# Kernel tuning notes

Measured on AMD Instinct MI355X. Metric: run time of the kernel, lower is better.

Reference implementation:

```python
import jax, jax.numpy as jnp
import numpy as np

DILATIONS = [1, 2, 4]


def _lstm_cell(x, h, c, W_ih, W_hh, b_ih, b_hh):
    # PyTorch LSTMCell: gates in i, f, g, o order
    gates = x @ W_ih.T + b_ih + h @ W_hh.T + b_hh
    i, f, g, o = jnp.split(gates, 4, axis=-1)
    c_new = jax.nn.sigmoid(f) * c + jax.nn.sigmoid(i) * jnp.tanh(g)
    h_new = jax.nn.sigmoid(o) * jnp.tanh(c_new)
    return h_new, c_new


def _drnn_forward(x, params):
    B, T, _ = x.shape
    H = params[0][1].shape[1]
    L = len(params)
    # static per-(t, layer) update mask from dilations
    masks = jnp.asarray(
        np.array([[t % d == 0 for d in DILATIONS] for t in range(T)], dtype=bool)
    )  # [T, L]

    hs0 = tuple(jnp.zeros((B, H), x.dtype) for _ in range(L))
    cs0 = tuple(jnp.zeros((B, H), x.dtype) for _ in range(L))

    def step(carry, inp):
        hs, cs = carry
        x_t, m = inp  # x_t: [B, F], m: [L] bool
        hs = list(hs)
        cs = list(cs)
        for l, (Wi, Wh, bi, bh) in enumerate(params):
            inp_l = x_t if l == 0 else hs[l - 1]
            h_new, c_new = _lstm_cell(inp_l, hs[l], cs[l], Wi, Wh, bi, bh)
            hs[l] = jnp.where(m[l], h_new, hs[l])
            cs[l] = jnp.where(m[l], c_new, cs[l])
        return (tuple(hs), tuple(cs)), hs[-1]

    _, ys = jax.lax.scan(step, (hs0, cs0), (jnp.swapaxes(x, 0, 1), masks))
    return jnp.swapaxes(ys, 0, 1)  # [B, T, H]


def setup_inputs() -> dict:
    key = jax.random.key(0)
    ks = jax.random.split(key, 16)
    B, T, F, H = 128, 1024, 128, 256
    k = 1.0 / np.sqrt(H)  # torch LSTMCell init scale

    def u(kk, shape):
        return jax.random.uniform(kk, shape, jnp.float32, -k, k)

    inp = {"x": jax.random.normal(ks[0], (B, T, F), jnp.float32)}
    in_sizes = [F, H, H]
    ki = 1
    for l in range(3):
        inp[f"W_ih{l}"] = u(ks[ki], (4 * H, in_sizes[l])); ki += 1
        inp[f"W_hh{l}"] = u(ks[ki], (4 * H, H)); ki += 1
        inp[f"b_ih{l}"] = u(ks[ki], (4 * H,)); ki += 1
        inp[f"b_hh{l}"] = u(ks[ki], (4 * H,)); ki += 1
    return inp


def reference(x, W_ih0, W_hh0, b_ih0, b_hh0,
              W_ih1, W_hh1, b_ih1, b_hh1,
              W_ih2, W_hh2, b_ih2, b_hh2):
    params = [
        (W_ih0, W_hh0, b_ih0, b_hh0),
        (W_ih1, W_hh1, b_ih1, b_hh1),
        (W_ih2, W_hh2, b_ih2, b_hh2),
    ]
    return _drnn_forward(x, params)
```

## Files before the change

kernel.cpp:

```cpp
#include <hip/hip_runtime.h>
#include <hip/hip_fp16.h>
#include <stdint.h>
#include <stddef.h>


typedef _Float16 f16;
typedef _Float16 v2h __attribute__((ext_vector_type(2)));
typedef _Float16 v8h __attribute__((ext_vector_type(8)));
typedef __fp16 h2_raw __attribute__((ext_vector_type(2)));
typedef __fp16 h8_raw __attribute__((ext_vector_type(8)));
typedef float v4f __attribute__((ext_vector_type(4)));
typedef unsigned long long u64;

#define DEVINL static __device__ __forceinline__

DEVINL float sigm(float x) { return 1.0f / (1.0f + __expf(-x)); }
DEVINL float tanh_(float x) {
  x = fminf(fmaxf(x, -15.0f), 15.0f);
  float e = __expf(-2.0f * x);
  return (1.0f - e) / (1.0f + e);
}
DEVINL v2h pack2(float a, float b) {
  return __builtin_bit_cast(v2h, __builtin_amdgcn_cvt_pkrtz(a, b));
}
DEVINL v2h bcast_pair(v2h v, int l) {
  int i = __builtin_bit_cast(int, v);
  i = __builtin_amdgcn_readlane(i, l);
  return __builtin_bit_cast(v2h, i);
}
DEVINL float fdot2(v2h a, v2h b, float c) {
  return __builtin_amdgcn_fdot2(__builtin_bit_cast(h2_raw, a),
                                __builtin_bit_cast(h2_raw, b), c, false);
}
DEVINL v4f mfma_16x16x32(v8h a, v8h b, v4f c) {
  return __builtin_amdgcn_mfma_f32_16x16x32_f16(__builtin_bit_cast(h8_raw, a),
                                                __builtin_bit_cast(h8_raw, b), c,
                                                0, 0, 0);
}


__global__ void k_cvt_x(const float2* __restrict__ src, v2h* __restrict__ dst, int n2) {
  int i = blockIdx.x * blockDim.x + threadIdx.x;
  int st = gridDim.x * blockDim.x;
  for (; i < n2; i += st) {
    float2 v = src[i];
    dst[i] = pack2(v.x, v.y);
  }
}

__global__ void k_prep_w(const float* __restrict__ wih0, const float* __restrict__ whh0,
                         const float* __restrict__ wih1, const float* __restrict__ whh1,
                         const float* __restrict__ wih2, const float* __restrict__ whh2,
                         const float* __restrict__ bi0, const float* __restrict__ bh0,
                         const float* __restrict__ bi1, const float* __restrict__ bh1,
                         const float* __restrict__ bi2, const float* __restrict__ bh2,
                         f16* wih0f, f16* whh0f, f16* wih1f, f16* whh1f,
                         f16* wih2f, f16* whh2f,
                         float* bias0, float* bias1, float* bias2) {
  int i = blockIdx.x * blockDim.x + threadIdx.x;
  if (i < 131072) wih0f[i] = (f16)wih0[i];
  whh0f[i] = (f16)whh0[i];
  wih1f[i] = (f16)wih1[i];
  whh1f[i] = (f16)whh1[i];
  wih2f[i] = (f16)wih2[i];
  whh2f[i] = (f16)whh2[i];
  if (i < 1024) {
    bias0[i] = bi0[i] + bh0[i];
    bias1[i] = bi1[i] + bh1[i];
    bias2[i] = bi2[i] + bh2[i];
  }
}


template <int K>
__launch_bounds__(256)
__global__ void k_gemm(const f16* __restrict__ A, int Tb, int t0,
                       const f16* __restrict__ W, const float* __restrict__ bias,
                       f16* __restrict__ G) {
  constexpr int LDK = K + 8;
  __shared__ f16 As[64 * LDK];
  int b = blockIdx.x >> 2, tb = blockIdx.x & 3;
  const f16* Ablk = A + ((size_t)b * Tb + t0 + tb * 64) * K;
  int tid = threadIdx.x;

  constexpr int NV = 64 * K / 8;
  const uint4* src = (const uint4*)Ablk;
  for (int i = tid; i < NV; i += 256) {
    int e = i * 8;
    int r = e / K, c0 = e % K;
    *(uint4*)&As[r * LDK + c0] = src[i];
  }
  __syncthreads();

  int wave = tid >> 6, lane = tid & 63;
  int lm = lane & 15, lk = (lane >> 4) * 8;

  v8h af[K / 32];
#pragma unroll
  for (int kc = 0; kc < K / 32; ++kc)
    af[kc] = *(const v8h*)&As[(wave * 16 + lm) * LDK + kc * 32 + lk];

  size_t grow0 = (size_t)b * 256 + tb * 64 + wave * 16;
  for (int nt = 0; nt < 64; ++nt) {
    v4f acc = {0.0f, 0.0f, 0.0f, 0.0f};
    const f16* Wrow = W + (size_t)(nt * 16 + lm) * K + lk;
#pragma unroll
    for (int kc = 0; kc < K / 32; ++kc) {
      v8h bf = *(const v8h*)(Wrow + kc * 32);
      acc = mfma_16x16x32(af[kc], bf, acc);
    }
    float bv = bias[nt * 16 + lm];
#pragma unroll
    for (int r = 0; r < 4; ++r) {
      int m = (lane >> 4) * 4 + r;
      G[(grow0 + m) * 1024 + nt * 16 + lm] = (f16)(acc[r] + bv);
    }
  }
}


template <int LAYER>
__launch_bounds__(512, 2)
__global__ void k_rec(const f16* __restrict__ G,
                      const f16* __restrict__ Whh,
                      int t0, int steps,
                      f16* __restrict__ Hout, float* __restrict__ y,
                      float* __restrict__ hstate, float* __restrict__ cstate,
                      u64* hxw) {
  int blk = blockIdx.x;
  int b = blk >> 1, half = blk & 1;
  int tid = threadIdx.x;
  int lane = tid & 63;
  int g = tid >> 7, j = tid & 127;
  int col = g * 256 + half * 128 + j;

  __shared__ float gbuf[512];
  __shared__ uint32_t hbufw[64];

  v2h w0[64], w1[64];
  {
    const v8h* wown = (const v8h*)(Whh + (size_t)col * 256 + half * 128);
    const v8h* woth = (const v8h*)(Whh + (size_t)col * 256 + (1 - half) * 128);
#pragma unroll
    for (int i = 0; i < 16; ++i) {
      v8h qa = wown[i], qb = woth[i];
#pragma unroll
      for (int p = 0; p < 4; ++p) {
        v2h ta, tb;
        ta[0] = qa[2 * p]; ta[1] = qa[2 * p + 1];
        tb[0] = qb[2 * p]; tb[1] = qb[2 * p + 1];
        w0[i * 4 + p] = ta;
        w1[i * 4 + p] = tb;
      }
    }
  }

  u64* myw = hxw + (size_t)(b * 2 + half) * 128;
  const u64* pw = hxw + (size_t)(b * 2 + (1 - half)) * 128;

  float c_st = 0.0f, last_h = 0.0f;
  v2h hp_own = pack2(0.0f, 0.0f), hp_oth = pack2(0.0f, 0.0f);

  if (t0 > 0) {
    float2 a = *(const float2*)&hstate[b * 256 + half * 128 + 2 * lane];
    hp_own = pack2(a.x, a.y);
    if (tid < 128) {
      last_h = hstate[b * 256 + half * 128 + tid];
      c_st = cstate[b * 256 + half * 128 + tid];
    }
  }

  const f16* Gp = G + (size_t)b * 256 * 1024 + col;
  float gcur = (float)Gp[0];

  for (int s = 0; s < steps; ++s) {
    int t = t0 + s;

    const u64* pwp = pw + (((t - 1) & 1) << 6) + lane;
    u64 wp = 0;
    if (t > 0)
      wp = __hip_atomic_load(pwp, __ATOMIC_RELAXED, __HIP_MEMORY_SCOPE_AGENT);
    float gnext = (s + 1 < steps) ? (float)Gp[(size_t)(s + 1) << 10] : 0.0f;

    float acc = gcur;
#pragma unroll
    for (int kk = 0; kk < 64; ++kk)
      acc = fdot2(w0[kk], bcast_pair(hp_own, kk), acc);

    if (t > 0) {
      while ((int)(wp >> 32) < t)
        wp = __hip_atomic_load(pwp, __ATOMIC_RELAXED, __HIP_MEMORY_SCOPE_AGENT);
      hp_oth = __builtin_bit_cast(v2h, (uint32_t)wp);
    }

#pragma unroll
    for (int kk = 0; kk < 64; ++kk)
      acc = fdot2(w1[kk], bcast_pair(hp_oth, kk), acc);

    gbuf[tid] = acc;
    __syncthreads();

    if (tid < 128) {
      float iv = sigm(gbuf[tid]);
      float fv = sigm(gbuf[tid + 128]);
      float gv = tanh_(gbuf[tid + 256]);
      float ov = sigm(gbuf[tid + 384]);
      c_st = fv * c_st + iv * gv;
      float hnew = ov * tanh_(c_st);
      last_h = hnew;
      float hn1 = __shfl_down(hnew, 1, 64);
      if ((tid & 1) == 0) {
        uint32_t pk = __builtin_bit_cast(uint32_t, pack2(hnew, hn1));
        u64 wv = ((u64)(uint32_t)(t + 1) << 32) | (u64)pk;
        __hip_atomic_store(&myw[((t & 1) << 6) + (tid >> 1)], wv,
                           __ATOMIC_RELAXED, __HIP_MEMORY_SCOPE_AGENT);
        hbufw[tid >> 1] = pk;
      }
      if (LAYER == 0) {
        if ((t & 1) == 0)
          Hout[((size_t)b * 512 + (t >> 1)) * 256 + half * 128 + tid] = (f16)hnew;
      } else if (LAYER == 1) {
        if ((t & 1) == 0)
          Hout[((size_t)b * 256 + (t >> 1)) * 256 + half * 128 + tid] = (f16)hnew;
      } else {
        size_t base = ((size_t)b * 1024 + (size_t)t * 4) * 256 + half * 128 + tid;
        y[base] = hnew;
        y[base + 256] = hnew;
        y[base + 512] = hnew;
        y[base + 768] = hnew;
      }
    }
    __syncthreads();
    hp_own = __builtin_bit_cast(v2h, hbufw[lane]);
    gcur = gnext;
  }

  if (tid < 128) {
    hstate[b * 256 + half * 128 + tid] = last_h;
    cstate[b * 256 + half * 128 + tid] = c_st;
  }
}


extern "C" void kernel_launch(void* const* d_in, const int* in_sizes, int n_in,
                              void* d_out, int out_size, void* d_ws, size_t ws_size,
                              hipStream_t stream) {
  const float* x = (const float*)d_in[0];
  const float* wih[3] = {(const float*)d_in[1], (const float*)d_in[5], (const float*)d_in[9]};
  const float* whh[3] = {(const float*)d_in[2], (const float*)d_in[6], (const float*)d_in[10]};
  const float* bi[3] = {(const float*)d_in[3], (const float*)d_in[7], (const float*)d_in[11]};
  const float* bh[3] = {(const float*)d_in[4], (const float*)d_in[8], (const float*)d_in[12]};
  float* y = (float*)d_out;

  char* p = (char*)d_ws;
  f16* Xf = (f16*)p;        p += (size_t)16777216 * 2;
  f16* Wih0f = (f16*)p;     p += (size_t)131072 * 2;
  f16* Whh0f = (f16*)p;     p += (size_t)262144 * 2;
  f16* Wih1f = (f16*)p;     p += (size_t)262144 * 2;
  f16* Whh1f = (f16*)p;     p += (size_t)262144 * 2;
  f16* Wih2f = (f16*)p;     p += (size_t)262144 * 2;
  f16* Whh2f = (f16*)p;     p += (size_t)262144 * 2;
  float* bias0 = (float*)p; p += 4096;
  float* bias1 = (float*)p; p += 4096;
  float* bias2 = (float*)p; p += 4096;
  f16* Gbuf = (f16*)p;      p += (size_t)32768 * 1024 * 2;
  f16* H0e = (f16*)p;       p += (size_t)128 * 512 * 256 * 2;
  f16* H1q = (f16*)p;       p += (size_t)128 * 256 * 256 * 2;
  float* hstate = (float*)p; p += (size_t)128 * 256 * 4;
  float* cstate = (float*)p; p += (size_t)128 * 256 * 4;
  u64* hxw0 = (u64*)p;      p += (size_t)128 * 2 * 128 * 8;
  u64* hxw1 = (u64*)p;      p += (size_t)128 * 2 * 128 * 8;
  u64* hxw2 = (u64*)p;      p += (size_t)128 * 2 * 128 * 8;

  k_cvt_x<<<4096, 256, 0, stream>>>((const float2*)x, (v2h*)Xf, 8388608);
  k_prep_w<<<1024, 256, 0, stream>>>(wih[0], whh[0], wih[1], whh[1], wih[2], whh[2],
                                     bi[0], bh[0], bi[1], bh[1], bi[2], bh[2],
                                     Wih0f, Whh0f, Wih1f, Whh1f, Wih2f, Whh2f,
                                     bias0, bias1, bias2);

  for (int c = 0; c < 4; ++c) {
    k_gemm<128><<<512, 256, 0, stream>>>(Xf, 1024, c * 256, Wih0f, bias0, Gbuf);
    k_rec<0><<<256, 512, 0, stream>>>(Gbuf, Whh0f, c * 256, 256, H0e, nullptr,
                                      hstate, cstate, hxw0);
  }
  for (int c = 0; c < 2; ++c) {
    k_gemm<256><<<512, 256, 0, stream>>>(H0e, 512, c * 256, Wih1f, bias1, Gbuf);
    k_rec<1><<<256, 512, 0, stream>>>(Gbuf, Whh1f, c * 256, 256, H1q, nullptr,
                                      hstate, cstate, hxw1);
  }
  k_gemm<256><<<512, 256, 0, stream>>>(H1q, 256, 0, Wih2f, bias2, Gbuf);
  k_rec<2><<<256, 512, 0, stream>>>(Gbuf, Whh2f, 0, 256, nullptr, y,
                                    hstate, cstate, hxw2);
}
```

Measured before the change: 4.740 ms.

## Compute LSTM cell redundantly per wave to drop second barrier per step

```diff
diff --git a/kernel.cpp b/kernel.cpp
--- a/kernel.cpp
+++ b/kernel.cpp
@@ -128,14 +128,14 @@
                       float* __restrict__ hstate, float* __restrict__ cstate,
                       u64* hxw) {
   int blk = blockIdx.x;
-  int b = blk >> 1, half = blk & 1;
+  int b = blk & 127, half = blk >> 7;
   int tid = threadIdx.x;
   int lane = tid & 63;
+  int wv = tid >> 6;
   int g = tid >> 7, j = tid & 127;
   int col = g * 256 + half * 128 + j;
 
-  __shared__ float gbuf[512];
-  __shared__ uint32_t hbufw[64];
+  __shared__ float gbuf[2][512];
 
   v2h w0[64], w1[64];
   {
@@ -158,16 +158,15 @@
   u64* myw = hxw + (size_t)(b * 2 + half) * 128;
   const u64* pw = hxw + (size_t)(b * 2 + (1 - half)) * 128;
 
-  float c_st = 0.0f, last_h = 0.0f;
+  float c0 = 0.0f, c1 = 0.0f, h0 = 0.0f, h1 = 0.0f;
   v2h hp_own = pack2(0.0f, 0.0f), hp_oth = pack2(0.0f, 0.0f);
 
   if (t0 > 0) {
-    float2 a = *(const float2*)&hstate[b * 256 + half * 128 + 2 * lane];
+    int sbase = b * 256 + half * 128 + 2 * lane;
+    float2 a = *(const float2*)&hstate[sbase];
+    float2 cc = *(const float2*)&cstate[sbase];
     hp_own = pack2(a.x, a.y);
-    if (tid < 128) {
-      last_h = hstate[b * 256 + half * 128 + tid];
-      c_st = cstate[b * 256 + half * 128 + tid];
-    }
+    h0 = a.x; h1 = a.y; c0 = cc.x; c1 = cc.y;
   }
 
   const f16* Gp = G + (size_t)b * 256 * 1024 + col;
@@ -182,10 +181,14 @@
       wp = __hip_atomic_load(pwp, __ATOMIC_RELAXED, __HIP_MEMORY_SCOPE_AGENT);
     float gnext = (s + 1 < steps) ? (float)Gp[(size_t)(s + 1) << 10] : 0.0f;
 
-    float acc = gcur;
-#pragma unroll
-    for (int kk = 0; kk < 64; ++kk)
-      acc = fdot2(w0[kk], bcast_pair(hp_own, kk), acc);
+    float a0 = gcur, a1 = 0.0f, a2 = 0.0f, a3 = 0.0f;
+#pragma unroll
+    for (int kk = 0; kk < 64; kk += 4) {
+      a0 = fdot2(w0[kk + 0], bcast_pair(hp_own, kk + 0), a0);
+      a1 = fdot2(w0[kk + 1], bcast_pair(hp_own, kk + 1), a1);
+      a2 = fdot2(w0[kk + 2], bcast_pair(hp_own, kk + 2), a2);
+      a3 = fdot2(w0[kk + 3], bcast_pair(hp_own, kk + 3), a3);
+    }
 
     if (t > 0) {
       while ((int)(wp >> 32) < t)
@@ -194,50 +197,62 @@
     }
 
 #pragma unroll
-    for (int kk = 0; kk < 64; ++kk)
-      acc = fdot2(w1[kk], bcast_pair(hp_oth, kk), acc);
-
-    gbuf[tid] = acc;
+    for (int kk = 0; kk < 64; kk += 4) {
+      a0 = fdot2(w1[kk + 0], bcast_pair(hp_oth, kk + 0), a0);
+      a1 = fdot2(w1[kk + 1], bcast_pair(hp_oth, kk + 1), a1);
+      a2 = fdot2(w1[kk + 2], bcast_pair(hp_oth, kk + 2), a2);
+      a3 = fdot2(w1[kk + 3], bcast_pair(hp_oth, kk + 3), a3);
+    }
+
+    gbuf[t & 1][tid] = (a0 + a1) + (a2 + a3);
     __syncthreads();
 
-    if (tid < 128) {
-      float iv = sigm(gbuf[tid]);
-      float fv = sigm(gbuf[tid + 128]);
-      float gv = tanh_(gbuf[tid + 256]);
-      float ov = sigm(gbuf[tid + 384]);
-      c_st = fv * c_st + iv * gv;
-      float hnew = ov * tanh_(c_st);
-      last_h = hnew;
-      float hn1 = __shfl_down(hnew, 1, 64);
-      if ((tid & 1) == 0) {
-        uint32_t pk = __builtin_bit_cast(uint32_t, pack2(hnew, hn1));
-        u64 wv = ((u64)(uint32_t)(t + 1) << 32) | (u64)pk;
-        __hip_atomic_store(&myw[((t & 1) << 6) + (tid >> 1)], wv,
-                           __ATOMIC_RELAXED, __HIP_MEMORY_SCOPE_AGENT);
-        hbufw[tid >> 1] = pk;
+    const float* gb = gbuf[t & 1];
+    float2 gi = *(const float2*)&gb[2 * lane];
+    float2 gf = *(const float2*)&gb[2 * lane + 128];
+    float2 gg = *(const float2*)&gb[2 * lane + 256];
+    float2 go = *(const float2*)&gb[2 * lane + 384];
+    c0 = sigm(gf.x) * c0 + sigm(gi.x) * tanh_(gg.x);
+    c1 = sigm(gf.y) * c1 + sigm(gi.y) * tanh_(gg.y);
+    h0 = sigm(go.x) * tanh_(c0);
+    h1 = sigm(go.y) * tanh_(c1);
+    hp_own = pack2(h0, h1);
+
+    if (wv == 0) {
+      uint32_t pk = __builtin_bit_cast(uint32_t, hp_own);
+      u64 word = ((u64)(uint32_t)(t + 1) << 32) | (u64)pk;
+      __hip_atomic_store(&myw[((t & 1) << 6) + lane], word,
+                         __ATOMIC_RELAXED, __HIP_MEMORY_SCOPE_AGENT);
+    }
+    if (LAYER == 0) {
+      if (wv == 1 && (t & 1) == 0) {
+        v2h hr; hr[0] = (f16)h0; hr[1] = (f16)h1;
+        *(uint32_t*)&Hout[((size_t)b * 512 + (t >> 1)) * 256 + half * 128 + 2 * lane] =
+            __builtin_bit_cast(uint32_t, hr);
       }
-      if (LAYER == 0) {
-        if ((t & 1) == 0)
-          Hout[((size_t)b * 512 + (t >> 1)) * 256 + half * 128 + tid] = (f16)hnew;
-      } else if (LAYER == 1) {
-        if ((t & 1) == 0)
-          Hout[((size_t)b * 256 + (t >> 1)) * 256 + half * 128 + tid] = (f16)hnew;
-      } else {
-        size_t base = ((size_t)b * 1024 + (size_t)t * 4) * 256 + half * 128 + tid;
-        y[base] = hnew;
-        y[base + 256] = hnew;
-        y[base + 512] = hnew;
-        y[base + 768] = hnew;
+    } else if (LAYER == 1) {
+      if (wv == 1 && (t & 1) == 0) {
+        v2h hr; hr[0] = (f16)h0; hr[1] = (f16)h1;
+        *(uint32_t*)&Hout[((size_t)b * 256 + (t >> 1)) * 256 + half * 128 + 2 * lane] =
+            __builtin_bit_cast(uint32_t, hr);
       }
-    }
-    __syncthreads();
-    hp_own = __builtin_bit_cast(v2h, hbufw[lane]);
+    } else {
+      if (wv >= 2 && wv < 6) {
+        size_t base = ((size_t)b * 1024 + (size_t)t * 4 + (wv - 2)) * 256 +
+                      half * 128 + 2 * lane;
+        float2 hv; hv.x = h0; hv.y = h1;
+        *(float2*)&y[base] = hv;
+      }
+    }
     gcur = gnext;
   }
 
-  if (tid < 128) {
-    hstate[b * 256 + half * 128 + tid] = last_h;
-    cstate[b * 256 + half * 128 + tid] = c_st;
+  if (wv == 0) {
+    int sbase = b * 256 + half * 128 + 2 * lane;
+    float2 hv; hv.x = h0; hv.y = h1;
+    float2 cv; cv.x = c0; cv.y = c1;
+    *(float2*)&hstate[sbase] = hv;
+    *(float2*)&cstate[sbase] = cv;
   }
 }
 
```

After: 4.697 ms. Within noise of the previous version (-0.9%).

## Batch recurrent step over 8 sequences per block using MFMA instead of fdot2

Applied to the files above, without the earlier changes.

```diff
diff --git a/kernel.cpp b/kernel.cpp
--- a/kernel.cpp
+++ b/kernel.cpp
@@ -22,15 +22,6 @@
 }
 DEVINL v2h pack2(float a, float b) {
   return __builtin_bit_cast(v2h, __builtin_amdgcn_cvt_pkrtz(a, b));
-}
-DEVINL v2h bcast_pair(v2h v, int l) {
-  int i = __builtin_bit_cast(int, v);
-  i = __builtin_amdgcn_readlane(i, l);
-  return __builtin_bit_cast(v2h, i);
-}
-DEVINL float fdot2(v2h a, v2h b, float c) {
-  return __builtin_amdgcn_fdot2(__builtin_bit_cast(h2_raw, a),
-                                __builtin_bit_cast(h2_raw, b), c, false);
 }
 DEVINL v4f mfma_16x16x32(v8h a, v8h b, v4f c) {
   return __builtin_amdgcn_mfma_f32_16x16x32_f16(__builtin_bit_cast(h8_raw, a),
@@ -128,117 +119,149 @@
                       float* __restrict__ hstate, float* __restrict__ cstate,
                       u64* hxw) {
   int blk = blockIdx.x;
-  int b = blk >> 1, half = blk & 1;
+  int g = blk & 15, half = blk >> 4;
   int tid = threadIdx.x;
   int lane = tid & 63;
-  int g = tid >> 7, j = tid & 127;
-  int col = g * 256 + half * 128 + j;
-
-  __shared__ float gbuf[512];
-  __shared__ uint32_t hbufw[64];
-
-  v2h w0[64], w1[64];
+  int wv = tid >> 6;
+
+  int q = wv & 3, cs = wv >> 2;
+  int colbase = q * 256 + half * 128 + cs * 64;
+  int arow = lane & 15;
+  int kq = (lane >> 4) * 8;
+
+  int bl = wv, p = lane;
+  int b = g * 8 + bl;
+
+  __shared__ __align__(16) f16 hbuf[16][264];
+  __shared__ float gq[4][8][132];
+
+  v8h wf[32];
+#pragma unroll
+  for (int nt = 0; nt < 4; ++nt)
+#pragma unroll
+    for (int kt = 0; kt < 8; ++kt)
+      wf[nt * 8 + kt] =
+          *(const v8h*)&Whh[(size_t)(colbase + nt * 16 + arow) * 256 + kt * 32 + kq];
+
   {
-    const v8h* wown = (const v8h*)(Whh + (size_t)col * 256 + half * 128);
-    const v8h* woth = (const v8h*)(Whh + (size_t)col * 256 + (1 - half) * 128);
-#pragma unroll
-    for (int i = 0; i < 16; ++i) {
-      v8h qa = wown[i], qb = woth[i];
-#pragma unroll
-      for (int p = 0; p < 4; ++p) {
-        v2h ta, tb;
-        ta[0] = qa[2 * p]; ta[1] = qa[2 * p + 1];
-        tb[0] = qb[2 * p]; tb[1] = qb[2 * p + 1];
-        w0[i * 4 + p] = ta;
-        w1[i * 4 + p] = tb;
-      }
-    }
-  }
-
-  u64* myw = hxw + (size_t)(b * 2 + half) * 128;
-  const u64* pw = hxw + (size_t)(b * 2 + (1 - half)) * 128;
-
-  float c_st = 0.0f, last_h = 0.0f;
-  v2h hp_own = pack2(0.0f, 0.0f), hp_oth = pack2(0.0f, 0.0f);
-
+    uint32_t* hz = (uint32_t*)&hbuf[0][0];
+    for (int i = tid; i < 16 * 264 / 2; i += 512) hz[i] = 0u;
+  }
+  __syncthreads();
+
+  float c0 = 0.0f, c1 = 0.0f, h0f = 0.0f, h1f = 0.0f;
   if (t0 > 0) {
-    float2 a = *(const float2*)&hstate[b * 256 + half * 128 + 2 * lane];
-    hp_own = pack2(a.x, a.y);
-    if (tid < 128) {
-      last_h = hstate[b * 256 + half * 128 + tid];
-      c_st = cstate[b * 256 + half * 128 + tid];
-    }
-  }
-
-  const f16* Gp = G + (size_t)b * 256 * 1024 + col;
-  float gcur = (float)Gp[0];
+    for (int w = tid; w < 1024; w += 512) {
+      int rb = w >> 7, kp = w & 127;
+      float2 hv = *(const float2*)&hstate[(size_t)(g * 8 + rb) * 256 + 2 * kp];
+      *(uint32_t*)&hbuf[rb][2 * kp] = __builtin_bit_cast(uint32_t, pack2(hv.x, hv.y));
+    }
+    float2 cv = *(const float2*)&cstate[(size_t)b * 256 + half * 128 + 2 * p];
+    c0 = cv.x;
+    c1 = cv.y;
+  }
+  __syncthreads();
+
+  u64* myw = hxw + (size_t)(g * 2 + half) * 1024;
+  const u64* pw = hxw + (size_t)(g * 2 + (1 - half)) * 1024;
+
+  const f16* Gc = G + (size_t)b * 256 * 1024 + half * 128 + 2 * p;
+  uint32_t gv[4], gn[4];
+#pragma unroll
+  for (int j = 0; j < 4; ++j) gv[j] = *(const uint32_t*)&Gc[j * 256];
 
   for (int s = 0; s < steps; ++s) {
     int t = t0 + s;
-
-    const u64* pwp = pw + (((t - 1) & 1) << 6) + lane;
-    u64 wp = 0;
-    if (t > 0)
-      wp = __hip_atomic_load(pwp, __ATOMIC_RELAXED, __HIP_MEMORY_SCOPE_AGENT);
-    float gnext = (s + 1 < steps) ? (float)Gp[(size_t)(s + 1) << 10] : 0.0f;
-
-    float acc = gcur;
-#pragma unroll
-    for (int kk = 0; kk < 64; ++kk)
-      acc = fdot2(w0[kk], bcast_pair(hp_own, kk), acc);
-
-    if (t > 0) {
-      while ((int)(wp >> 32) < t)
+    int par = t & 1;
+
+    v4f acc[4] = {};
+#pragma unroll
+    for (int kt = 0; kt < 8; ++kt) {
+      v8h a = *(const v8h*)&hbuf[arow][kt * 32 + kq];
+#pragma unroll
+      for (int nt = 0; nt < 4; ++nt)
+        acc[nt] = mfma_16x16x32(a, wf[nt * 8 + kt], acc[nt]);
+    }
+    if (lane < 32) {
+      int r0 = (lane >> 4) * 4;
+      int d0 = cs * 64 + (lane & 15);
+#pragma unroll
+      for (int nt = 0; nt < 4; ++nt)
+#pragma unroll
+        for (int r = 0; r < 4; ++r)
+          gq[q][r0 + r][d0 + nt * 16] = acc[nt][r];
+    }
+    if (s + 1 < steps) {
+#pragma unroll
+      for (int j = 0; j < 4; ++j)
+        gn[j] = *(const uint32_t*)&Gc[(size_t)(s + 1) * 1024 + j * 256];
+    }
+    __syncthreads();
+
+    const u64* pwp = &pw[(size_t)par * 512 + bl * 64 + p];
+    u64 wp = __hip_atomic_load(pwp, __ATOMIC_RELAXED, __HIP_MEMORY_SCOPE_AGENT);
+
+    float2 zi = *(const float2*)&gq[0][bl][2 * p];
+    float2 zf = *(const float2*)&gq[1][bl][2 * p];
+    float2 zg = *(const float2*)&gq[2][bl][2 * p];
+    float2 zo = *(const float2*)&gq[3][bl][2 * p];
+    v2h G0 = __builtin_bit_cast(v2h, gv[0]);
+    v2h G1 = __builtin_bit_cast(v2h, gv[1]);
+    v2h G2 = __builtin_bit_cast(v2h, gv[2]);
+    v2h G3 = __builtin_bit_cast(v2h, gv[3]);
+
+    float i0 = sigm(zi.x + (float)G0[0]), i1 = sigm(zi.y + (float)G0[1]);
+    float f0 = sigm(zf.x + (float)G1[0]), f1 = sigm(zf.y + (float)G1[1]);
+    float g0 = tanh_(zg.x + (float)G2[0]), g1 = tanh_(zg.y + (float)G2[1]);
+    float o0 = sigm(zo.x + (float)G3[0]), o1 = sigm(zo.y + (float)G3[1]);
+    c0 = f0 * c0 + i0 * g0;
+    c1 = f1 * c1 + i1 * g1;
+    h0f = o0 * tanh_(c0);
+    h1f = o1 * tanh_(c1);
+
+    uint32_t hp = __builtin_bit_cast(uint32_t, pack2(h0f, h1f));
+    u64 word = ((u64)(uint32_t)(t + 1) << 32) | (u64)hp;
+    __hip_atomic_store(&myw[(size_t)par * 512 + bl * 64 + p], word,
+                       __ATOMIC_RELAXED, __HIP_MEMORY_SCOPE_AGENT);
+    *(uint32_t*)&hbuf[bl][half * 128 + 2 * p] = hp;
+
+    if (LAYER == 0) {
+      if ((t & 1) == 0) {
+        v2h hr; hr[0] = (f16)h0f; hr[1] = (f16)h1f;
+        *(uint32_t*)&Hout[((size_t)b * 512 + (t >> 1)) * 256 + half * 128 + 2 * p] =
+            __builtin_bit_cast(uint32_t, hr);
+      }
+    } else if (LAYER == 1) {
+      if ((t & 1) == 0) {
+        v2h hr; hr[0] = (f16)h0f; hr[1] = (f16)h1f;
+        *(uint32_t*)&Hout[((size_t)b * 256 + (t >> 1)) * 256 + half * 128 + 2 * p] =
+            __builtin_bit_cast(uint32_t, hr);
+      }
+    } else {
+      size_t base = ((size_t)b * 1024 + (size_t)t * 4) * 256 + half * 128 + 2 * p;
+      float2 hv; hv.x = h0f; hv.y = h1f;
+      *(float2*)&y[base] = hv;
+      *(float2*)&y[base + 256] = hv;
+      *(float2*)&y[base + 512] = hv;
+      *(float2*)&y[base + 768] = hv;
+    }
+
+    if (s + 1 < steps) {
+      while ((int)(wp >> 32) < t + 1)
         wp = __hip_atomic_load(pwp, __ATOMIC_RELAXED, __HIP_MEMORY_SCOPE_AGENT);
-      hp_oth = __builtin_bit_cast(v2h, (uint32_t)wp);
-    }
-
-#pragma unroll
-    for (int kk = 0; kk < 64; ++kk)
-      acc = fdot2(w1[kk], bcast_pair(hp_oth, kk), acc);
-
-    gbuf[tid] = acc;
+      *(uint32_t*)&hbuf[bl][(1 - half) * 128 + 2 * p] = (uint32_t)wp;
+    }
     __syncthreads();
 
-    if (tid < 128) {
-      float iv = sigm(gbuf[tid]);
-      float fv = sigm(gbuf[tid + 128]);
-      float gv = tanh_(gbuf[tid + 256]);
-      float ov = sigm(gbuf[tid + 384]);
-      c_st = fv * c_st + iv * gv;
-      float hnew = ov * tanh_(c_st);
-      last_h = hnew;
-      float hn1 = __shfl_down(hnew, 1, 64);
-      if ((tid & 1) == 0) {
-        uint32_t pk = __builtin_bit_cast(uint32_t, pack2(hnew, hn1));
-        u64 wv = ((u64)(uint32_t)(t + 1) << 32) | (u64)pk;
-        __hip_atomic_store(&myw[((t & 1) << 6) + (tid >> 1)], wv,
-                           __ATOMIC_RELAXED, __HIP_MEMORY_SCOPE_AGENT);
-        hbufw[tid >> 1] = pk;
-      }
-      if (LAYER == 0) {
-        if ((t & 1) == 0)
-          Hout[((size_t)b * 512 + (t >> 1)) * 256 + half * 128 + tid] = (f16)hnew;
-      } else if (LAYER == 1) {
-        if ((t & 1) == 0)
-          Hout[((size_t)b * 256 + (t >> 1)) * 256 + half * 128 + tid] = (f16)hnew;
-      } else {
-        size_t base = ((size_t)b * 1024 + (size_t)t * 4) * 256 + half * 128 + tid;
-        y[base] = hnew;
-        y[base + 256] = hnew;
-        y[base + 512] = hnew;
-        y[base + 768] = hnew;
-      }
-    }
-    __syncthreads();
-    hp_own = __builtin_bit_cast(v2h, hbufw[lane]);
-    gcur = gnext;
-  }
-
-  if (tid < 128) {
-    hstate[b * 256 + half * 128 + tid] = last_h;
-    cstate[b * 256 + half * 128 + tid] = c_st;
-  }
+#pragma unroll
+    for (int j = 0; j < 4; ++j) gv[j] = gn[j];
+  }
+
+  size_t sb = (size_t)b * 256 + half * 128 + 2 * p;
+  float2 hv; hv.x = h0f; hv.y = h1f;
+  float2 cv; cv.x = c0; cv.y = c1;
+  *(float2*)&hstate[sb] = hv;
+  *(float2*)&cstate[sb] = cv;
 }
 
 
@@ -268,9 +291,9 @@
   f16* H1q = (f16*)p;       p += (size_t)128 * 256 * 256 * 2;
   float* hstate = (float*)p; p += (size_t)128 * 256 * 4;
   float* cstate = (float*)p; p += (size_t)128 * 256 * 4;
-  u64* hxw0 = (u64*)p;      p += (size_t)128 * 2 * 128 * 8;
-  u64* hxw1 = (u64*)p;      p += (size_t)128 * 2 * 128 * 8;
-  u64* hxw2 = (u64*)p;      p += (size_t)128 * 2 * 128 * 8;
+  u64* hxw0 = (u64*)p;      p += (size_t)16 * 2 * 1024 * 8;
+  u64* hxw1 = (u64*)p;      p += (size_t)16 * 2 * 1024 * 8;
+  u64* hxw2 = (u64*)p;      p += (size_t)16 * 2 * 1024 * 8;
 
   k_cvt_x<<<4096, 256, 0, stream>>>((const float2*)x, (v2h*)Xf, 8388608);
   k_prep_w<<<1024, 256, 0, stream>>>(wih[0], whh[0], wih[1], whh[1], wih[2], whh[2],
@@ -280,15 +303,15 @@
 
   for (int c = 0; c < 4; ++c) {
     k_gemm<128><<<512, 256, 0, stream>>>(Xf, 1024, c * 256, Wih0f, bias0, Gbuf);
-    k_rec<0><<<256, 512, 0, stream>>>(Gbuf, Whh0f, c * 256, 256, H0e, nullptr,
-                                      hstate, cstate, hxw0);
+    k_rec<0><<<32, 512, 0, stream>>>(Gbuf, Whh0f, c * 256, 256, H0e, nullptr,
+                                     hstate, cstate, hxw0);
   }
   for (int c = 0; c < 2; ++c) {
     k_gemm<256><<<512, 256, 0, stream>>>(H0e, 512, c * 256, Wih1f, bias1, Gbuf);
-    k_rec<1><<<256, 512, 0, stream>>>(Gbuf, Whh1f, c * 256, 256, H1q, nullptr,
-                                      hstate, cstate, hxw1);
+    k_rec<1><<<32, 512, 0, stream>>>(Gbuf, Whh1f, c * 256, 256, H1q, nullptr,
+                                     hstate, cstate, hxw1);
   }
   k_gemm<256><<<512, 256, 0, stream>>>(H1q, 256, 0, Wih2f, bias2, Gbuf);
-  k_rec<2><<<256, 512, 0, stream>>>(Gbuf, Whh2f, 0, 256, nullptr, y,
-                                    hstate, cstate, hxw2);
-}
+  k_rec<2><<<32, 512, 0, stream>>>(Gbuf, Whh2f, 0, 256, nullptr, y,
+                                   hstate, cstate, hxw2);
+}
```

Result: faster. 4.501 ms (-5.1%).

## Batch recurrent step across 8 sequences per block using MFMA with register/LDS-resident weights

Applied to the files above, without the earlier changes.

```diff
diff --git a/kernel.cpp b/kernel.cpp
--- a/kernel.cpp
+++ b/kernel.cpp
@@ -20,17 +20,8 @@
   float e = __expf(-2.0f * x);
   return (1.0f - e) / (1.0f + e);
 }
-DEVINL v2h pack2(float a, float b) {
-  return __builtin_bit_cast(v2h, __builtin_amdgcn_cvt_pkrtz(a, b));
-}
-DEVINL v2h bcast_pair(v2h v, int l) {
-  int i = __builtin_bit_cast(int, v);
-  i = __builtin_amdgcn_readlane(i, l);
-  return __builtin_bit_cast(v2h, i);
-}
-DEVINL float fdot2(v2h a, v2h b, float c) {
-  return __builtin_amdgcn_fdot2(__builtin_bit_cast(h2_raw, a),
-                                __builtin_bit_cast(h2_raw, b), c, false);
+DEVINL uint32_t pk2(float a, float b) {
+  return __builtin_bit_cast(uint32_t, __builtin_amdgcn_cvt_pkrtz(a, b));
 }
 DEVINL v4f mfma_16x16x32(v8h a, v8h b, v4f c) {
   return __builtin_amdgcn_mfma_f32_16x16x32_f16(__builtin_bit_cast(h8_raw, a),
@@ -38,13 +29,25 @@
                                                 0, 0, 0);
 }
 
-
-__global__ void k_cvt_x(const float2* __restrict__ src, v2h* __restrict__ dst, int n2) {
+DEVINL void wg_barrier() {
+  __builtin_amdgcn_sched_barrier(0);
+  asm volatile("s_waitcnt lgkmcnt(0)" ::: "memory");
+  __builtin_amdgcn_s_barrier();
+  asm volatile("" ::: "memory");
+  __builtin_amdgcn_sched_barrier(0);
+}
+
+DEVINL int hb_off(int par, int row, int c) {
+  return par * 4096 + row * 512 + ((c ^ (row << 2)) << 4);
+}
+
+
+__global__ void k_cvt_x(const float2* __restrict__ src, uint32_t* __restrict__ dst, int n2) {
   int i = blockIdx.x * blockDim.x + threadIdx.x;
   int st = gridDim.x * blockDim.x;
   for (; i < n2; i += st) {
     float2 v = src[i];
-    dst[i] = pack2(v.x, v.y);
+    dst[i] = pk2(v.x, v.y);
   }
 }
 
@@ -120,124 +123,177 @@
 
 
 template <int LAYER>
-__launch_bounds__(512, 2)
+__launch_bounds__(512, 1)
 __global__ void k_rec(const f16* __restrict__ G,
                       const f16* __restrict__ Whh,
                       int t0, int steps,
                       f16* __restrict__ Hout, float* __restrict__ y,
-                      float* __restrict__ hstate, float* __restrict__ cstate,
-                      u64* hxw) {
-  int blk = blockIdx.x;
-  int b = blk >> 1, half = blk & 1;
+                      float* __restrict__ hstate, float* __restrict__ cstate) {
+  int g = blockIdx.x;
   int tid = threadIdx.x;
-  int lane = tid & 63;
-  int g = tid >> 7, j = tid & 127;
-  int col = g * 256 + half * 128 + j;
-
-  __shared__ float gbuf[512];
-  __shared__ uint32_t hbufw[64];
-
-  v2h w0[64], w1[64];
+  int lane = tid & 63, w = tid >> 6;
+  int q = w >> 1, dh = w & 1;
+  int arow = lane & 15, s4 = lane >> 4;
+  int bt = w;
+  int b = g * 8 + bt;
+
+  __shared__ __align__(16) f16 wlds[8][14][64][8];
+  __shared__ __align__(16) f16 hbuf[2][8][256];
+  __shared__ __align__(16) float gq[4][8][264];
+
+  v8h wr[8][6];
+  v8h wr6, wr7;
   {
-    const v8h* wown = (const v8h*)(Whh + (size_t)col * 256 + half * 128);
-    const v8h* woth = (const v8h*)(Whh + (size_t)col * 256 + (1 - half) * 128);
-#pragma unroll
-    for (int i = 0; i < 16; ++i) {
-      v8h qa = wown[i], qb = woth[i];
-#pragma unroll
-      for (int p = 0; p < 4; ++p) {
-        v2h ta, tb;
-        ta[0] = qa[2 * p]; ta[1] = qa[2 * p + 1];
-        tb[0] = qb[2 * p]; tb[1] = qb[2 * p + 1];
-        w0[i * 4 + p] = ta;
-        w1[i * 4 + p] = tb;
+    const f16* wp = Whh + (size_t)(q * 256 + dh * 128 + arow) * 256;
+#pragma unroll
+    for (int ct = 0; ct < 8; ++ct) {
+      const v8h* row = (const v8h*)(wp + (size_t)ct * 16 * 256);
+#pragma unroll
+      for (int kt = 0; kt < 6; ++kt) wr[ct][kt] = row[kt * 4 + s4];
+    }
+    const v8h* row0 = (const v8h*)wp;
+    wr6 = row0[6 * 4 + s4];
+    wr7 = row0[7 * 4 + s4];
+#pragma unroll
+    for (int ct = 1; ct < 8; ++ct) {
+      const v8h* row = (const v8h*)(wp + (size_t)ct * 16 * 256);
+#pragma unroll
+      for (int kt = 6; kt < 8; ++kt)
+        *(v8h*)&wlds[w][(ct - 1) * 2 + (kt - 6)][lane][0] = row[kt * 4 + s4];
+    }
+  }
+
+  if (tid < 256) {
+    int row = tid >> 5, c = tid & 31;
+    uint4 pk = {0u, 0u, 0u, 0u};
+    if (t0 > 0) {
+      const float4* hs = (const float4*)&hstate[(size_t)(g * 8 + row) * 256 + c * 8];
+      float4 a = hs[0], bq = hs[1];
+      pk.x = pk2(a.x, a.y);  pk.y = pk2(a.z, a.w);
+      pk.z = pk2(bq.x, bq.y); pk.w = pk2(bq.z, bq.w);
+    }
+    *(uint4*)((char*)hbuf + hb_off(0, row, c)) = pk;
+  }
+  float c0 = 0.f, c1 = 0.f, c2 = 0.f, c3 = 0.f;
+  if (t0 > 0) {
+    float4 cc = *(const float4*)&cstate[(size_t)b * 256 + 4 * lane];
+    c0 = cc.x; c1 = cc.y; c2 = cc.z; c3 = cc.w;
+  }
+  float h0 = 0.f, h1 = 0.f, h2 = 0.f, h3 = 0.f;
+
+  const f16* Gb = G + (size_t)b * 262144 + 4 * lane;
+  uint2 gv[4];
+#pragma unroll
+  for (int qg = 0; qg < 4; ++qg)
+    gv[qg] = *(const uint2*)(Gb + qg * 256);
+
+  __syncthreads();
+
+  for (int s = 0; s < steps; ++s) {
+    int p = s & 1;
+    int t = t0 + s;
+
+#pragma unroll
+    for (int pass = 0; pass < 2; ++pass) {
+      v4f acc[4] = {{0.f, 0.f, 0.f, 0.f}, {0.f, 0.f, 0.f, 0.f},
+                    {0.f, 0.f, 0.f, 0.f}, {0.f, 0.f, 0.f, 0.f}};
+#pragma unroll
+      for (int kt = 0; kt < 8; ++kt) {
+        v8h a = *(const v8h*)((const char*)hbuf + hb_off(p, arow & 7, kt * 4 + s4));
+#pragma unroll
+        for (int c4 = 0; c4 < 4; ++c4) {
+          const int ct = pass * 4 + c4;
+          v8h bf;
+          if (kt < 6) {
+            bf = wr[ct][kt];
+          } else if (ct == 0) {
+            bf = (kt == 6) ? wr6 : wr7;
+          } else {
+            bf = *(const v8h*)&wlds[w][(ct - 1) * 2 + (kt - 6)][lane][0];
+          }
+          acc[c4] = mfma_16x16x32(a, bf, acc[c4]);
+        }
       }
-    }
-  }
-
-  u64* myw = hxw + (size_t)(b * 2 + half) * 128;
-  const u64* pw = hxw + (size_t)(b * 2 + (1 - half)) * 128;
-
-  float c_st = 0.0f, last_h = 0.0f;
-  v2h hp_own = pack2(0.0f, 0.0f), hp_oth = pack2(0.0f, 0.0f);
-
-  if (t0 > 0) {
-    float2 a = *(const float2*)&hstate[b * 256 + half * 128 + 2 * lane];
-    hp_own = pack2(a.x, a.y);
-    if (tid < 128) {
-      last_h = hstate[b * 256 + half * 128 + tid];
-      c_st = cstate[b * 256 + half * 128 + tid];
-    }
-  }
-
-  const f16* Gp = G + (size_t)b * 256 * 1024 + col;
-  float gcur = (float)Gp[0];
-
-  for (int s = 0; s < steps; ++s) {
-    int t = t0 + s;
-
-    const u64* pwp = pw + (((t - 1) & 1) << 6) + lane;
-    u64 wp = 0;
-    if (t > 0)
-      wp = __hip_atomic_load(pwp, __ATOMIC_RELAXED, __HIP_MEMORY_SCOPE_AGENT);
-    float gnext = (s + 1 < steps) ? (float)Gp[(size_t)(s + 1) << 10] : 0.0f;
-
-    float acc = gcur;
-#pragma unroll
-    for (int kk = 0; kk < 64; ++kk)
-      acc = fdot2(w0[kk], bcast_pair(hp_own, kk), acc);
-
-    if (t > 0) {
-      while ((int)(wp >> 32) < t)
-        wp = __hip_atomic_load(pwp, __ATOMIC_RELAXED, __HIP_MEMORY_SCOPE_AGENT);
-      hp_oth = __builtin_bit_cast(v2h, (uint32_t)wp);
-    }
-
-#pragma unroll
-    for (int kk = 0; kk < 64; ++kk)
-      acc = fdot2(w1[kk], bcast_pair(hp_oth, kk), acc);
-
-    gbuf[tid] = acc;
-    __syncthreads();
-
-    if (tid < 128) {
-      float iv = sigm(gbuf[tid]);
-      float fv = sigm(gbuf[tid + 128]);
-      float gv = tanh_(gbuf[tid + 256]);
-      float ov = sigm(gbuf[tid + 384]);
-      c_st = fv * c_st + iv * gv;
-      float hnew = ov * tanh_(c_st);
-      last_h = hnew;
-      float hn1 = __shfl_down(hnew, 1, 64);
-      if ((tid & 1) == 0) {
-        uint32_t pk = __builtin_bit_cast(uint32_t, pack2(hnew, hn1));
-        u64 wv = ((u64)(uint32_t)(t + 1) << 32) | (u64)pk;
-        __hip_atomic_store(&myw[((t & 1) << 6) + (tid >> 1)], wv,
-                           __ATOMIC_RELAXED, __HIP_MEMORY_SCOPE_AGENT);
-        hbufw[tid >> 1] = pk;
+      if (s4 < 2) {
+        int r0 = s4 * 4;
+#pragma unroll
+        for (int c4 = 0; c4 < 4; ++c4)
+#pragma unroll
+          for (int r = 0; r < 4; ++r)
+            gq[q][r0 + r][dh * 128 + (pass * 4 + c4) * 16 + arow] = acc[c4][r];
       }
+    }
+    wg_barrier();
+
+    {
+      float4 zi = *(const float4*)&gq[0][bt][4 * lane];
+      float4 zf = *(const float4*)&gq[1][bt][4 * lane];
+      float4 zg = *(const float4*)&gq[2][bt][4 * lane];
+      float4 zo = *(const float4*)&gq[3][bt][4 * lane];
+      v2h gia = __builtin_bit_cast(v2h, gv[0].x), gib = __builtin_bit_cast(v2h, gv[0].y);
+      v2h gfa = __builtin_bit_cast(v2h, gv[1].x), gfb = __builtin_bit_cast(v2h, gv[1].y);
+      v2h gga = __builtin_bit_cast(v2h, gv[2].x), ggb = __builtin_bit_cast(v2h, gv[2].y);
+      v2h goa = __builtin_bit_cast(v2h, gv[3].x), gob = __builtin_bit_cast(v2h, gv[3].y);
+
+      float i0 = sigm(zi.x + (float)gia[0]), i1 = sigm(zi.y + (float)gia[1]);
+      float i2 = sigm(zi.z + (float)gib[0]), i3 = sigm(zi.w + (float)gib[1]);
+      float f0 = sigm(zf.x + (float)gfa[0]), f1 = sigm(zf.y + (float)gfa[1]);
+      float f2 = sigm(zf.z + (float)gfb[0]), f3 = sigm(zf.w + (float)gfb[1]);
+      float g0 = tanh_(zg.x + (float)gga[0]), g1 = tanh_(zg.y + (float)gga[1]);
+      float g2 = tanh_(zg.z + (float)ggb[0]), g3 = tanh_(zg.w + (float)ggb[1]);
+      float o0 = sigm(zo.x + (float)goa[0]), o1 = sigm(zo.y + (float)goa[1]);
+      float o2 = sigm(zo.z + (float)gob[0]), o3 = sigm(zo.w + (float)gob[1]);
+      c0 = f0 * c0 + i0 * g0;  c1 = f1 * c1 + i1 * g1;
+      c2 = f2 * c2 + i2 * g2;  c3 = f3 * c3 + i3 * g3;
+      h0 = o0 * tanh_(c0);  h1 = o1 * tanh_(c1);
+      h2 = o2 * tanh_(c2);  h3 = o3 * tanh_(c3);
+
+      uint2 hp; hp.x = pk2(h0, h1); hp.y = pk2(h2, h3);
+      *(uint2*)((char*)hbuf + hb_off(p ^ 1, bt, lane >> 1) + (lane & 1) * 8) = hp;
+
       if (LAYER == 0) {
-        if ((t & 1) == 0)
-          Hout[((size_t)b * 512 + (t >> 1)) * 256 + half * 128 + tid] = (f16)hnew;
+        if ((t & 1) == 0) {
+          uint2 hr;
+          hr.x = (uint32_t)__builtin_bit_cast(uint16_t, (f16)h0) |
+                 ((uint32_t)__builtin_bit_cast(uint16_t, (f16)h1) << 16);
+          hr.y = (uint32_t)__builtin_bit_cast(uint16_t, (f16)h2) |
+                 ((uint32_t)__builtin_bit_cast(uint16_t, (f16)h3) << 16);
+          *(uint2*)&Hout[((size_t)b * 512 + (t >> 1)) * 256 + 4 * lane] = hr;
+        }
       } else if (LAYER == 1) {
-        if ((t & 1) == 0)
-          Hout[((size_t)b * 256 + (t >> 1)) * 256 + half * 128 + tid] = (f16)hnew;
+        if ((t & 1) == 0) {
+          uint2 hr;
+          hr.x = (uint32_t)__builtin_bit_cast(uint16_t, (f16)h0) |
+                 ((uint32_t)__builtin_bit_cast(uint16_t, (f16)h1) << 16);
+          hr.y = (uint32_t)__builtin_bit_cast(uint16_t, (f16)h2) |
+                 ((uint32_t)__builtin_bit_cast(uint16_t, (f16)h3) << 16);
+          *(uint2*)&Hout[((size_t)b * 256 + (t >> 1)) * 256 + 4 * lane] = hr;
+        }
       } else {
-        size_t base = ((size_t)b * 1024 + (size_t)t * 4) * 256 + half * 128 + tid;
-        y[base] = hnew;
-        y[base + 256] = hnew;
-        y[base + 512] = hnew;
-        y[base + 768] = hnew;
+        size_t base = ((size_t)b * 1024 + (size_t)t * 4) * 256 + 4 * lane;
+        float4 hv; hv.x = h0; hv.y = h1; hv.z = h2; hv.w = h3;
+        *(float4*)&y[base] = hv;
+        *(float4*)&y[base + 256] = hv;
+        *(float4*)&y[base + 512] = hv;
+        *(float4*)&y[base + 768] = hv;
       }
-    }
-    __syncthreads();
-    hp_own = __builtin_bit_cast(v2h, hbufw[lane]);
-    gcur = gnext;
-  }
-
-  if (tid < 128) {
-    hstate[b * 256 + half * 128 + tid] = last_h;
-    cstate[b * 256 + half * 128 + tid] = c_st;
+
+      if (s + 1 < steps) {
+        const f16* Gs = Gb + (size_t)(s + 1) * 1024;
+#pragma unroll
+        for (int qg = 0; qg < 4; ++qg)
+          gv[qg] = *(const uint2*)(Gs + qg * 256);
+      }
+    }
+    wg_barrier();
+  }
+
+  {
+    size_t sb = (size_t)b * 256 + 4 * lane;
+    float4 hv; hv.x = h0; hv.y = h1; hv.z = h2; hv.w = h3;
+    float4 cv; cv.x = c0; cv.y = c1; cv.z = c2; cv.w = c3;
+    *(float4*)&hstate[sb] = hv;
+    *(float4*)&cstate[sb] = cv;
   }
 }
 
@@ -268,11 +324,8 @@
   f16* H1q = (f16*)p;       p += (size_t)128 * 256 * 256 * 2;
   float* hstate = (float*)p; p += (size_t)128 * 256 * 4;
   float* cstate = (float*)p; p += (size_t)128 * 256 * 4;
-  u64* hxw0 = (u64*)p;      p += (size_t)128 * 2 * 128 * 8;
-  u64* hxw1 = (u64*)p;      p += (size_t)128 * 2 * 128 * 8;
-  u64* hxw2 = (u64*)p;      p += (size_t)128 * 2 * 128 * 8;
-
-  k_cvt_x<<<4096, 256, 0, stream>>>((const float2*)x, (v2h*)Xf, 8388608);
+
+  k_cvt_x<<<4096, 256, 0, stream>>>((const float2*)x, (uint32_t*)Xf, 8388608);
   k_prep_w<<<1024, 256, 0, stream>>>(wih[0], whh[0], wih[1], whh[1], wih[2], whh[2],
                                      bi[0], bh[0], bi[1], bh[1], bi[2], bh[2],
                                      Wih0f, Whh0f, Wih1f, Whh1f, Wih2f, Whh2f,
@@ -280,15 +333,15 @@
 
   for (int c = 0; c < 4; ++c) {
     k_gemm<128><<<512, 256, 0, stream>>>(Xf, 1024, c * 256, Wih0f, bias0, Gbuf);
-    k_rec<0><<<256, 512, 0, stream>>>(Gbuf, Whh0f, c * 256, 256, H0e, nullptr,
-                                      hstate, cstate, hxw0);
+    k_rec<0><<<16, 512, 0, stream>>>(Gbuf, Whh0f, c * 256, 256, H0e, nullptr,
+                                     hstate, cstate);
   }
   for (int c = 0; c < 2; ++c) {
     k_gemm<256><<<512, 256, 0, stream>>>(H0e, 512, c * 256, Wih1f, bias1, Gbuf);
-    k_rec<1><<<256, 512, 0, stream>>>(Gbuf, Whh1f, c * 256, 256, H1q, nullptr,
-                                      hstate, cstate, hxw1);
+    k_rec<1><<<16, 512, 0, stream>>>(Gbuf, Whh1f, c * 256, 256, H1q, nullptr,
+                                     hstate, cstate);
   }
   k_gemm<256><<<512, 256, 0, stream>>>(H1q, 256, 0, Wih2f, bias2, Gbuf);
-  k_rec<2><<<256, 512, 0, stream>>>(Gbuf, Whh2f, 0, 256, nullptr, y,
-                                    hstate, cstate, hxw2);
-}
+  k_rec<2><<<16, 512, 0, stream>>>(Gbuf, Whh2f, 0, 256, nullptr, y,
+                                   hstate, cstate);
+}
```

After: 8.784 ms. 85.3% more time.
